# Kernel tuning notes

Measured on AMD Instinct MI355X. Metric: run time of the kernel, lower is better.

Reference implementation:

```python
import jax, jax.numpy as jnp
import numpy as np

B, S, D = 8, 2048, 1024  # batch, seq_len, d_model == output_size


def setup_inputs() -> dict:
    key = jax.random.key(0)
    ks = jax.random.split(key, 10)
    scale = 1.0 / np.sqrt(D)
    return {
        "query": jax.random.normal(ks[0], (B, S, D), jnp.float32),
        "key": jax.random.normal(ks[1], (B, S, D), jnp.float32),
        "value": jax.random.normal(ks[2], (B, S, D), jnp.float32),
        "mask": jax.random.randint(ks[3], (B, S), 0, 2, jnp.int32),
        "Wq": jax.random.uniform(ks[4], (D, D), jnp.float32, -scale, scale),
        "bq": jax.random.uniform(ks[5], (D,), jnp.float32, -scale, scale),
        "Wk": jax.random.uniform(ks[6], (D, D), jnp.float32, -scale, scale),
        "bk": jax.random.uniform(ks[7], (D,), jnp.float32, -scale, scale),
        "Wv": jax.random.uniform(ks[8], (D, D), jnp.float32, -scale, scale),
        "bv": jax.random.uniform(ks[9], (D,), jnp.float32, -scale, scale),
    }


def reference(query, key, value, mask, Wq, bq, Wk, bk, Wv, bv):
    # Linear projections (torch Linear: x @ W.T + b)
    Q = jnp.einsum("bsd,od->bso", query, Wq) + bq
    K = jnp.einsum("bsd,od->bso", key, Wk) + bk
    V = jnp.einsum("bsd,od->bso", value, Wv) + bv
    d_k = K.shape[-1]
    scores = jnp.einsum("bqd,bkd->bqk", Q, K) / jnp.sqrt(jnp.float32(d_k))
    # 2-D mask [B, S_k] -> broadcast over query positions; masked_fill(~mask, -inf)
    m = (mask != 0)[:, None, :]  # [B, 1, S_k]
    scores = jnp.where(m, scores, -jnp.inf)
    weights = jax.nn.softmax(scores, axis=-1)
    # dropout omitted (eval-mode / deterministic baseline)
    out = jnp.einsum("bqk,bkv->bqv", weights, V)
    return out
```

## Files before the change

kernel.cpp:

```cpp
#include <hip/hip_runtime.h>


#define BATCH 8
#define SEQ   2048
#define DM    1024

typedef __bf16 bf16x8 __attribute__((ext_vector_type(8)));
typedef float  f32x4  __attribute__((ext_vector_type(4)));
typedef unsigned short ushort8 __attribute__((ext_vector_type(8)));
typedef unsigned short ushort4v __attribute__((ext_vector_type(4)));

__device__ __forceinline__ unsigned short f2b(float f) {
    __bf16 h = (__bf16)f;
    return __builtin_bit_cast(unsigned short, h);
}

__device__ __forceinline__ void stage_async(const unsigned short* g,
                                            unsigned short* l) {
    __builtin_amdgcn_global_load_lds(
        (const __attribute__((address_space(1))) void*)g,
        (__attribute__((address_space(3))) void*)l, 16, 0, 0);
}

__device__ __forceinline__ void frag_mfma(const unsigned short* As,
                                          const unsigned short* Bs,
                                          f32x4 acc[4][4], int waveM, int waveN,
                                          int quad, int l16) {
    bf16x8 af[4], bf[4];
#pragma unroll
    for (int i = 0; i < 4; ++i)
        af[i] = *(const bf16x8*)(As + (waveM * 64 + i * 16 + l16) * 32 + quad * 8);
#pragma unroll
    for (int j = 0; j < 4; ++j)
        bf[j] = *(const bf16x8*)(Bs + (waveN * 64 + j * 16 + l16) * 32 + quad * 8);
#pragma unroll
    for (int i = 0; i < 4; ++i)
#pragma unroll
        for (int j = 0; j < 4; ++j)
            acc[i][j] = __builtin_amdgcn_mfma_f32_16x16x32_bf16(
                af[i], bf[j], acc[i][j], 0, 0, 0);
}

__global__ __launch_bounds__(256) void build_idx(
    const int* __restrict__ mask, int* __restrict__ idx,
    int* __restrict__ cnt, int* __restrict__ cntp) {
    const int b = blockIdx.x;
    const int* m = mask + b * SEQ;
    const int t = threadIdx.x;
    __shared__ int sums[256];
    int loc[8], s = 0;
#pragma unroll
    for (int u = 0; u < 8; ++u) { loc[u] = (m[t * 8 + u] != 0); s += loc[u]; }
    sums[t] = s;
    __syncthreads();
    for (int off = 1; off < 256; off <<= 1) {
        int v = (t >= off) ? sums[t - off] : 0;
        __syncthreads();
        sums[t] += v;
        __syncthreads();
    }
    int base = sums[t] - s;
#pragma unroll
    for (int u = 0; u < 8; ++u)
        if (loc[u]) idx[b * SEQ + base++] = t * 8 + u;
    if (t == 255) {
        cnt[b] = sums[255];
        cntp[b] = (sums[255] + 127) & ~127;
    }
}

__global__ void cast_bf16_all(const float* __restrict__ Wq,
                              const float* __restrict__ Wk,
                              const float* __restrict__ Wv,
                              unsigned short* __restrict__ wq,
                              unsigned short* __restrict__ wk,
                              unsigned short* __restrict__ wv) {
    const int p = blockIdx.x >> 9;
    const int lb = blockIdx.x & 511;
    const float* src = (p == 0) ? Wq : (p == 1) ? Wk : Wv;
    unsigned short* dst = (p == 0) ? wq : (p == 1) ? wk : wv;
    int i = lb * blockDim.x + threadIdx.x;
    const f32x4* s4 = (const f32x4*)src;
    f32x4 a = s4[2 * i], b = s4[2 * i + 1];
    ushort8 o;
    o[0] = f2b(a[0]); o[1] = f2b(a[1]); o[2] = f2b(a[2]); o[3] = f2b(a[3]);
    o[4] = f2b(b[0]); o[5] = f2b(b[1]); o[6] = f2b(b[2]); o[7] = f2b(b[3]);
    ((ushort8*)dst)[i] = o;
}

template <bool GATHER, bool TROUT>
__device__ __forceinline__ void proj_body(
    const float* __restrict__ X, const unsigned short* __restrict__ W,
    unsigned short* __restrict__ C, const float* __restrict__ bias,
    const int* __restrict__ idx, const int* __restrict__ cnt,
    const int* __restrict__ cntp, int bz, int i2,
    unsigned short* As, unsigned short* Bs) {
    const int n0 = (i2 & 7) * 128;
    const int m0 = (i2 >> 3) * 128;
    if (GATHER && m0 >= cntp[bz]) return;

    const int tid = threadIdx.x;
    const int wave = tid >> 6, lane = tid & 63;
    const int waveM = wave >> 1, waveN = wave & 1;
    const int quad = lane >> 4, l16 = lane & 15;

    f32x4 acc[4][4] = {};

    const int arow = tid >> 1;
    const int col0 = (tid & 1) * 16;
    const float* rp;
    if (GATHER) {
        const int gm = m0 + arow;
        rp = (gm < cnt[bz])
                 ? X + ((size_t)bz * SEQ + idx[bz * SEQ + gm]) * DM + col0
                 : nullptr;
    } else {
        rp = X + ((size_t)bz * SEQ + m0 + arow) * DM + col0;
    }
    unsigned short* lA = As + arow * 32 + col0;

    const int sr = lane >> 2, sc = (lane & 3) * 8;
    const unsigned short* gB = W + (size_t)(n0 + wave * 32 + sr) * DM + sc;
    unsigned short* lB = Bs + (wave * 32 + sr) * 32 + sc;

    const bool haveA = (!GATHER) || (rp != nullptr);
    f32x4 a0 = {}, a1 = {}, a2 = {}, a3 = {};
    if (haveA) {
        const f32x4* p4 = (const f32x4*)rp;
        a0 = p4[0]; a1 = p4[1]; a2 = p4[2]; a3 = p4[3];
    }

    for (int kt = 0; kt < DM; kt += 32) {
        stage_async(gB + kt, lB);
        stage_async(gB + kt + 16 * DM, lB + 16 * 32);
        ushort8 o0, o1;
        o0[0] = f2b(a0[0]); o0[1] = f2b(a0[1]); o0[2] = f2b(a0[2]); o0[3] = f2b(a0[3]);
        o0[4] = f2b(a1[0]); o0[5] = f2b(a1[1]); o0[6] = f2b(a1[2]); o0[7] = f2b(a1[3]);
        o1[0] = f2b(a2[0]); o1[1] = f2b(a2[1]); o1[2] = f2b(a2[2]); o1[3] = f2b(a2[3]);
        o1[4] = f2b(a3[0]); o1[5] = f2b(a3[1]); o1[6] = f2b(a3[2]); o1[7] = f2b(a3[3]);
        *(ushort8*)lA = o0;
        *(ushort8*)(lA + 8) = o1;
        if (haveA && kt + 32 < DM) {
            const f32x4* p4 = (const f32x4*)(rp + kt + 32);
            a0 = p4[0]; a1 = p4[1]; a2 = p4[2]; a3 = p4[3];
        }
        __syncthreads();
        frag_mfma(As, Bs, acc, waveM, waveN, quad, l16);
        __syncthreads();
    }

    if (!TROUT) {
        unsigned short* Cb = C + (size_t)bz * SEQ * DM;
#pragma unroll
        for (int i = 0; i < 4; ++i) {
            const int gmb = m0 + waveM * 64 + i * 16 + quad * 4;
#pragma unroll
            for (int j = 0; j < 4; ++j) {
                const int gn = n0 + waveN * 64 + j * 16 + l16;
                const float bv = bias[gn];
#pragma unroll
                for (int r = 0; r < 4; ++r)
                    Cb[(size_t)(gmb + r) * DM + gn] = f2b(acc[i][j][r] + bv);
            }
        }
    } else {
        unsigned short* Cb = C + (size_t)bz * (size_t)DM * SEQ;
#pragma unroll
        for (int i = 0; i < 4; ++i) {
            const int gmb = m0 + waveM * 64 + i * 16 + quad * 4;
#pragma unroll
            for (int j = 0; j < 4; ++j) {
                const int gn = n0 + waveN * 64 + j * 16 + l16;
                const float bv = bias[gn];
                ushort4v o;
#pragma unroll
                for (int r = 0; r < 4; ++r) o[r] = f2b(acc[i][j][r] + bv);
                *(ushort4v*)(Cb + (size_t)gn * SEQ + gmb) = o;
            }
        }
    }
}

__global__ __launch_bounds__(256) void proj_gemm_all(
    const float* __restrict__ q, const float* __restrict__ k,
    const float* __restrict__ v, const unsigned short* __restrict__ wq,
    const unsigned short* __restrict__ wk, const unsigned short* __restrict__ wv,
    unsigned short* __restrict__ Qp, unsigned short* __restrict__ Kc,
    unsigned short* __restrict__ Vt, const float* __restrict__ bq,
    const float* __restrict__ bk, const float* __restrict__ bv,
    const int* __restrict__ idx, const int* __restrict__ cnt,
    const int* __restrict__ cntp) {
    const int l = blockIdx.x + 8 * (blockIdx.y + 16 * blockIdx.z);
    const int p = l >> 10;
    const int bz = l & 7;
    const int i2 = (l & 1023) >> 3;

    __shared__ __align__(16) unsigned short As[128 * 32];
    __shared__ __align__(16) unsigned short Bs[128 * 32];

    if (p == 0)
        proj_body<false, false>(q, wq, Qp, bq, nullptr, nullptr, nullptr, bz, i2, As, Bs);
    else if (p == 1)
        proj_body<true, false>(k, wk, Kc, bk, idx, cnt, cntp, bz, i2, As, Bs);
    else
        proj_body<true, true>(v, wv, Vt, bv, idx, cnt, cntp, bz, i2, As, Bs);
}

__global__ __launch_bounds__(256) void scores_gemm(
    const unsigned short* __restrict__ Qp, const unsigned short* __restrict__ Kc,
    unsigned short* __restrict__ P, float* __restrict__ rowsum,
    const int* __restrict__ cnt, const int* __restrict__ cntp, float scale) {
    const int l = blockIdx.x + 16 * (blockIdx.y + 16 * blockIdx.z);
    const int bz = l & 7;
    const int i2 = l >> 3;
    const int n0 = (i2 & 15) * 128;
    const int m0 = (i2 >> 4) * 128;
    if (n0 >= cntp[bz]) return;

    const int tid = threadIdx.x;
    const int wave = tid >> 6, lane = tid & 63;
    const int waveM = wave >> 1, waveN = wave & 1;
    const int quad = lane >> 4, l16 = lane & 15;

    __shared__ __align__(16) unsigned short As[128 * 32];
    __shared__ __align__(16) unsigned short Bs[128 * 32];
    f32x4 acc[4][4] = {};

    const unsigned short* Ag = Qp + (size_t)bz * SEQ * DM;
    const unsigned short* Bg = Kc + (size_t)bz * SEQ * DM;
    const int sr = lane >> 2, sc = (lane & 3) * 8;
    const unsigned short* gA = Ag + (size_t)(m0 + wave * 32 + sr) * DM + sc;
    const unsigned short* gB = Bg + (size_t)(n0 + wave * 32 + sr) * DM + sc;
    unsigned short* lA = As + (wave * 32 + sr) * 32 + sc;
    unsigned short* lB = Bs + (wave * 32 + sr) * 32 + sc;

    for (int kt = 0; kt < DM; kt += 32) {
        stage_async(gA + kt, lA);
        stage_async(gA + kt + 16 * DM, lA + 16 * 32);
        stage_async(gB + kt, lB);
        stage_async(gB + kt + 16 * DM, lB + 16 * 32);
        __syncthreads();
        frag_mfma(As, Bs, acc, waveM, waveN, quad, l16);
        __syncthreads();
    }

    unsigned short* Cb = P + (size_t)bz * SEQ * SEQ;
    const int cn = cnt[bz];
#pragma unroll
    for (int i = 0; i < 4; ++i) {
        const int gmb = m0 + waveM * 64 + i * 16 + quad * 4;
        float rpart[4] = {0.f, 0.f, 0.f, 0.f};
#pragma unroll
        for (int j = 0; j < 4; ++j) {
            const int gn = n0 + waveN * 64 + j * 16 + l16;
            const float mv = (gn < cn) ? 1.0f : 0.0f;
#pragma unroll
            for (int r = 0; r < 4; ++r) {
                const float p = mv * __expf(acc[i][j][r] * scale);
                rpart[r] += p;
                Cb[(size_t)(gmb + r) * SEQ + gn] = f2b(p);
            }
        }
#pragma unroll
        for (int r = 0; r < 4; ++r) {
            float s = rpart[r];
            s += __shfl_xor(s, 1, 64);
            s += __shfl_xor(s, 2, 64);
            s += __shfl_xor(s, 4, 64);
            s += __shfl_xor(s, 8, 64);
            if (l16 == 0)
                atomicAdd(&rowsum[bz * SEQ + gmb + r], s);
        }
    }
}

__global__ __launch_bounds__(256) void pv_gemm(
    const unsigned short* __restrict__ P, const unsigned short* __restrict__ Vt,
    float* __restrict__ O, const float* __restrict__ rowsum,
    const int* __restrict__ cntp) {
    const int l = blockIdx.x + 8 * (blockIdx.y + 16 * blockIdx.z);
    const int bz = l & 7;
    const int i2 = l >> 3;
    const int n0 = (i2 & 7) * 128;
    const int m0 = (i2 >> 3) * 128;
    const int kend = cntp[bz];

    const int tid = threadIdx.x;
    const int wave = tid >> 6, lane = tid & 63;
    const int waveM = wave >> 1, waveN = wave & 1;
    const int quad = lane >> 4, l16 = lane & 15;

    __shared__ __align__(16) unsigned short As[128 * 32];
    __shared__ __align__(16) unsigned short Bs[128 * 32];
    f32x4 acc[4][4] = {};

    const unsigned short* Ag = P + (size_t)bz * SEQ * SEQ;
    const unsigned short* Bg = Vt + (size_t)bz * (size_t)DM * SEQ;
    const int sr = lane >> 2, sc = (lane & 3) * 8;
    const unsigned short* gA = Ag + (size_t)(m0 + wave * 32 + sr) * SEQ + sc;
    const unsigned short* gB = Bg + (size_t)(n0 + wave * 32 + sr) * SEQ + sc;
    unsigned short* lA = As + (wave * 32 + sr) * 32 + sc;
    unsigned short* lB = Bs + (wave * 32 + sr) * 32 + sc;

    for (int kt = 0; kt < kend; kt += 32) {
        stage_async(gA + kt, lA);
        stage_async(gA + kt + 16 * SEQ, lA + 16 * 32);
        stage_async(gB + kt, lB);
        stage_async(gB + kt + 16 * SEQ, lB + 16 * 32);
        __syncthreads();
        frag_mfma(As, Bs, acc, waveM, waveN, quad, l16);
        __syncthreads();
    }

    float* Cb = O + (size_t)bz * SEQ * DM;
#pragma unroll
    for (int i = 0; i < 4; ++i) {
        const int gmb = m0 + waveM * 64 + i * 16 + quad * 4;
        float inv[4];
#pragma unroll
        for (int r = 0; r < 4; ++r)
            inv[r] = 1.0f / rowsum[bz * SEQ + gmb + r];
#pragma unroll
        for (int j = 0; j < 4; ++j) {
            const int gn = n0 + waveN * 64 + j * 16 + l16;
#pragma unroll
            for (int r = 0; r < 4; ++r)
                Cb[(size_t)(gmb + r) * DM + gn] = acc[i][j][r] * inv[r];
        }
    }
}

extern "C" void kernel_launch(void* const* d_in, const int* in_sizes, int n_in,
                              void* d_out, int out_size, void* d_ws, size_t ws_size,
                              hipStream_t stream) {
    const float* query = (const float*)d_in[0];
    const float* key_  = (const float*)d_in[1];
    const float* value = (const float*)d_in[2];
    const int*   mask  = (const int*)d_in[3];
    const float* Wq = (const float*)d_in[4];
    const float* bq = (const float*)d_in[5];
    const float* Wk = (const float*)d_in[6];
    const float* bk = (const float*)d_in[7];
    const float* Wv = (const float*)d_in[8];
    const float* bv = (const float*)d_in[9];
    float* out = (float*)d_out;

    char* ws = (char*)d_ws;
    const size_t MB = 1024 * 1024;
    unsigned short* Qp    = (unsigned short*)(ws);
    unsigned short* Kc    = (unsigned short*)(ws + 32 * MB);
    unsigned short* Vtc   = (unsigned short*)(ws + 64 * MB);
    unsigned short* probs = (unsigned short*)(ws + 96 * MB);
    unsigned short* wq    = (unsigned short*)(ws + 160 * MB);
    unsigned short* wk    = (unsigned short*)(ws + 162 * MB);
    unsigned short* wv    = (unsigned short*)(ws + 164 * MB);
    float* rowsum = (float*)(ws + 166 * MB);
    int*   idx    = (int*)(ws + 166 * MB + 64 * 1024);
    int*   cnt    = (int*)(ws + 166 * MB + 128 * 1024);
    int*   cntp   = (int*)(ws + 166 * MB + 128 * 1024 + 64);

    hipMemsetAsync(rowsum, 0, (size_t)BATCH * SEQ * sizeof(float), stream);
    build_idx<<<BATCH, 256, 0, stream>>>(mask, idx, cnt, cntp);

    cast_bf16_all<<<1536, 256, 0, stream>>>(Wq, Wk, Wv, wq, wk, wv);

    proj_gemm_all<<<dim3(8, 16, 24), dim3(256), 0, stream>>>(
        query, key_, value, wq, wk, wv, Qp, Kc, Vtc, bq, bk, bv,
        idx, cnt, cntp);

    scores_gemm<<<dim3(16, 16, 8), dim3(256), 0, stream>>>(
        Qp, Kc, probs, rowsum, cnt, cntp, 0.03125f);

    pv_gemm<<<dim3(8, 16, 8), dim3(256), 0, stream>>>(
        probs, Vtc, out, rowsum, cntp);
}
```

Before: 440.6 us.

## Double-buffer LDS tiles in projection, scores and PV GEMM kernels

Each of the three GEMM kernels now keeps two LDS tile buffers. It issues the async global-to-LDS loads for the next K-slice before running MFMAs on the current slice, which drops one of the two barriers per iteration. This is meant to hide global load latency behind compute. The cost is double the LDS per block (32KB), which may reduce occupancy. Correctness depends on the single barrier also covering completion of the async loads.

```diff
diff --git a/kernel.cpp b/kernel.cpp
--- a/kernel.cpp
+++ b/kernel.cpp
@@ -94,7 +94,8 @@
     unsigned short* __restrict__ C, const float* __restrict__ bias,
     const int* __restrict__ idx, const int* __restrict__ cnt,
     const int* __restrict__ cntp, int bz, int i2,
-    unsigned short* As, unsigned short* Bs) {
+    unsigned short* As0, unsigned short* As1,
+    unsigned short* Bs0, unsigned short* Bs1) {
     const int n0 = (i2 & 7) * 128;
     const int m0 = (i2 >> 3) * 128;
     if (GATHER && m0 >= cntp[bz]) return;
@@ -117,36 +118,59 @@
     } else {
         rp = X + ((size_t)bz * SEQ + m0 + arow) * DM + col0;
     }
-    unsigned short* lA = As + arow * 32 + col0;
+    const int lAoff = arow * 32 + col0;
 
     const int sr = lane >> 2, sc = (lane & 3) * 8;
     const unsigned short* gB = W + (size_t)(n0 + wave * 32 + sr) * DM + sc;
-    unsigned short* lB = Bs + (wave * 32 + sr) * 32 + sc;
+    const int lBoff = (wave * 32 + sr) * 32 + sc;
 
     const bool haveA = (!GATHER) || (rp != nullptr);
+
     f32x4 a0 = {}, a1 = {}, a2 = {}, a3 = {};
     if (haveA) {
         const f32x4* p4 = (const f32x4*)rp;
         a0 = p4[0]; a1 = p4[1]; a2 = p4[2]; a3 = p4[3];
     }
-
-    for (int kt = 0; kt < DM; kt += 32) {
-        stage_async(gB + kt, lB);
-        stage_async(gB + kt + 16 * DM, lB + 16 * 32);
+    stage_async(gB, Bs0 + lBoff);
+    stage_async(gB + 16 * DM, Bs0 + lBoff + 16 * 32);
+    {
         ushort8 o0, o1;
         o0[0] = f2b(a0[0]); o0[1] = f2b(a0[1]); o0[2] = f2b(a0[2]); o0[3] = f2b(a0[3]);
         o0[4] = f2b(a1[0]); o0[5] = f2b(a1[1]); o0[6] = f2b(a1[2]); o0[7] = f2b(a1[3]);
         o1[0] = f2b(a2[0]); o1[1] = f2b(a2[1]); o1[2] = f2b(a2[2]); o1[3] = f2b(a2[3]);
         o1[4] = f2b(a3[0]); o1[5] = f2b(a3[1]); o1[6] = f2b(a3[2]); o1[7] = f2b(a3[3]);
-        *(ushort8*)lA = o0;
-        *(ushort8*)(lA + 8) = o1;
-        if (haveA && kt + 32 < DM) {
-            const f32x4* p4 = (const f32x4*)(rp + kt + 32);
-            a0 = p4[0]; a1 = p4[1]; a2 = p4[2]; a3 = p4[3];
-        }
+        *(ushort8*)(As0 + lAoff) = o0;
+        *(ushort8*)(As0 + lAoff + 8) = o1;
+    }
+    if (haveA) {
+        const f32x4* p4 = (const f32x4*)(rp + 32);
+        a0 = p4[0]; a1 = p4[1]; a2 = p4[2]; a3 = p4[3];
+    }
+    __syncthreads();
+
+    int cur = 0;
+    for (int kt = 0; kt < DM; kt += 32) {
+        const int nx = kt + 32;
+        if (nx < DM) {
+            unsigned short* Asn = cur ? As0 : As1;
+            unsigned short* Bsn = cur ? Bs0 : Bs1;
+            stage_async(gB + nx, Bsn + lBoff);
+            stage_async(gB + nx + 16 * DM, Bsn + lBoff + 16 * 32);
+            ushort8 o0, o1;
+            o0[0] = f2b(a0[0]); o0[1] = f2b(a0[1]); o0[2] = f2b(a0[2]); o0[3] = f2b(a0[3]);
+            o0[4] = f2b(a1[0]); o0[5] = f2b(a1[1]); o0[6] = f2b(a1[2]); o0[7] = f2b(a1[3]);
+            o1[0] = f2b(a2[0]); o1[1] = f2b(a2[1]); o1[2] = f2b(a2[2]); o1[3] = f2b(a2[3]);
+            o1[4] = f2b(a3[0]); o1[5] = f2b(a3[1]); o1[6] = f2b(a3[2]); o1[7] = f2b(a3[3]);
+            *(ushort8*)(Asn + lAoff) = o0;
+            *(ushort8*)(Asn + lAoff + 8) = o1;
+            if (haveA && nx + 32 < DM) {
+                const f32x4* p4 = (const f32x4*)(rp + nx + 32);
+                a0 = p4[0]; a1 = p4[1]; a2 = p4[2]; a3 = p4[3];
+            }
+        }
+        frag_mfma(cur ? As1 : As0, cur ? Bs1 : Bs0, acc, waveM, waveN, quad, l16);
         __syncthreads();
-        frag_mfma(As, Bs, acc, waveM, waveN, quad, l16);
-        __syncthreads();
+        cur ^= 1;
     }
 
     if (!TROUT) {
@@ -195,15 +219,18 @@
     const int bz = l & 7;
     const int i2 = (l & 1023) >> 3;
 
-    __shared__ __align__(16) unsigned short As[128 * 32];
-    __shared__ __align__(16) unsigned short Bs[128 * 32];
+    __shared__ __align__(16) unsigned short As[2][128 * 32];
+    __shared__ __align__(16) unsigned short Bs[2][128 * 32];
 
     if (p == 0)
-        proj_body<false, false>(q, wq, Qp, bq, nullptr, nullptr, nullptr, bz, i2, As, Bs);
+        proj_body<false, false>(q, wq, Qp, bq, nullptr, nullptr, nullptr, bz, i2,
+                                As[0], As[1], Bs[0], Bs[1]);
     else if (p == 1)
-        proj_body<true, false>(k, wk, Kc, bk, idx, cnt, cntp, bz, i2, As, Bs);
+        proj_body<true, false>(k, wk, Kc, bk, idx, cnt, cntp, bz, i2,
+                               As[0], As[1], Bs[0], Bs[1]);
     else
-        proj_body<true, true>(v, wv, Vt, bv, idx, cnt, cntp, bz, i2, As, Bs);
+        proj_body<true, true>(v, wv, Vt, bv, idx, cnt, cntp, bz, i2,
+                              As[0], As[1], Bs[0], Bs[1]);
 }
 
 __global__ __launch_bounds__(256) void scores_gemm(
@@ -222,8 +249,8 @@
     const int waveM = wave >> 1, waveN = wave & 1;
     const int quad = lane >> 4, l16 = lane & 15;
 
-    __shared__ __align__(16) unsigned short As[128 * 32];
-    __shared__ __align__(16) unsigned short Bs[128 * 32];
+    __shared__ __align__(16) unsigned short As[2][128 * 32];
+    __shared__ __align__(16) unsigned short Bs[2][128 * 32];
     f32x4 acc[4][4] = {};
 
     const unsigned short* Ag = Qp + (size_t)bz * SEQ * DM;
@@ -231,17 +258,29 @@
     const int sr = lane >> 2, sc = (lane & 3) * 8;
     const unsigned short* gA = Ag + (size_t)(m0 + wave * 32 + sr) * DM + sc;
     const unsigned short* gB = Bg + (size_t)(n0 + wave * 32 + sr) * DM + sc;
-    unsigned short* lA = As + (wave * 32 + sr) * 32 + sc;
-    unsigned short* lB = Bs + (wave * 32 + sr) * 32 + sc;
-
+    const int loff = (wave * 32 + sr) * 32 + sc;
+
+    stage_async(gA, As[0] + loff);
+    stage_async(gA + 16 * DM, As[0] + loff + 16 * 32);
+    stage_async(gB, Bs[0] + loff);
+    stage_async(gB + 16 * DM, Bs[0] + loff + 16 * 32);
+    __syncthreads();
+
+    int cur = 0;
     for (int kt = 0; kt < DM; kt += 32) {
-        stage_async(gA + kt, lA);
-        stage_async(gA + kt + 16 * DM, lA + 16 * 32);
-        stage_async(gB + kt, lB);
-        stage_async(gB + kt + 16 * DM, lB + 16 * 32);
+        const int nx = kt + 32;
+        if (nx < DM) {
+            unsigned short* Asn = cur ? As[0] : As[1];
+            unsigned short* Bsn = cur ? Bs[0] : Bs[1];
+            stage_async(gA + nx, Asn + loff);
+            stage_async(gA + nx + 16 * DM, Asn + loff + 16 * 32);
+            stage_async(gB + nx, Bsn + loff);
+            stage_async(gB + nx + 16 * DM, Bsn + loff + 16 * 32);
+        }
+        frag_mfma(cur ? As[1] : As[0], cur ? Bs[1] : Bs[0], acc,
+                  waveM, waveN, quad, l16);
         __syncthreads();
-        frag_mfma(As, Bs, acc, waveM, waveN, quad, l16);
-        __syncthreads();
+        cur ^= 1;
     }
 
     unsigned short* Cb = P + (size_t)bz * SEQ * SEQ;
@@ -290,8 +329,8 @@
     const int waveM = wave >> 1, waveN = wave & 1;
     const int quad = lane >> 4, l16 = lane & 15;
 
-    __shared__ __align__(16) unsigned short As[128 * 32];
-    __shared__ __align__(16) unsigned short Bs[128 * 32];
+    __shared__ __align__(16) unsigned short As[2][128 * 32];
+    __shared__ __align__(16) unsigned short Bs[2][128 * 32];
     f32x4 acc[4][4] = {};
 
     const unsigned short* Ag = P + (size_t)bz * SEQ * SEQ;
@@ -299,17 +338,29 @@
     const int sr = lane >> 2, sc = (lane & 3) * 8;
     const unsigned short* gA = Ag + (size_t)(m0 + wave * 32 + sr) * SEQ + sc;
     const unsigned short* gB = Bg + (size_t)(n0 + wave * 32 + sr) * SEQ + sc;
-    unsigned short* lA = As + (wave * 32 + sr) * 32 + sc;
-    unsigned short* lB = Bs + (wave * 32 + sr) * 32 + sc;
-
+    const int loff = (wave * 32 + sr) * 32 + sc;
+
+    stage_async(gA, As[0] + loff);
+    stage_async(gA + 16 * SEQ, As[0] + loff + 16 * 32);
+    stage_async(gB, Bs[0] + loff);
+    stage_async(gB + 16 * SEQ, Bs[0] + loff + 16 * 32);
+    __syncthreads();
+
+    int cur = 0;
     for (int kt = 0; kt < kend; kt += 32) {
-        stage_async(gA + kt, lA);
-        stage_async(gA + kt + 16 * SEQ, lA + 16 * 32);
-        stage_async(gB + kt, lB);
-        stage_async(gB + kt + 16 * SEQ, lB + 16 * 32);
+        const int nx = kt + 32;
+        if (nx < kend) {
+            unsigned short* Asn = cur ? As[0] : As[1];
+            unsigned short* Bsn = cur ? Bs[0] : Bs[1];
+            stage_async(gA + nx, Asn + loff);
+            stage_async(gA + nx + 16 * SEQ, Asn + loff + 16 * 32);
+            stage_async(gB + nx, Bsn + loff);
+            stage_async(gB + nx + 16 * SEQ, Bsn + loff + 16 * 32);
+        }
+        frag_mfma(cur ? As[1] : As[0], cur ? Bs[1] : Bs[0], acc,
+                  waveM, waveN, quad, l16);
         __syncthreads();
-        frag_mfma(As, Bs, acc, waveM, waveN, quad, l16);
-        __syncthreads();
+        cur ^= 1;
     }
 
     float* Cb = O + (size_t)bz * SEQ * DM;
```

Measured after the change: 444.4 us. Within noise of the previous version (+0.9%).
